# Kernel tuning notes

Hardware: AMD Instinct MI355X
Metric: run time of the kernel (lower is better)

Reference implementation:

```python
import jax, jax.numpy as jnp
import numpy as np

EPS = 0.01
H, W = 300, 400
WORLD_SCALE = 400.0


def setup_inputs() -> dict:
    key = jax.random.key(0)
    ks = jax.random.split(key, 8)
    N, B, D, HID = 200000, 2, 256, 256
    fx = fy = 300.0
    cx, cy = W / 2.0, H / 2.0
    z = jax.random.uniform(ks[0], (N,), minval=2.0, maxval=10.0)
    u = jax.random.uniform(ks[1], (N,), minval=0.0, maxval=float(W))
    v = jax.random.uniform(ks[2], (N,), minval=0.0, maxval=float(H))
    vert_pos = jnp.stack([(u - cx) / fx * z, (v - cy) / fy * z, z], axis=0)  # [3,N]
    target_pose = jnp.tile(jnp.eye(4, dtype=jnp.float32)[None], (B, 1, 1))
    K = jnp.array([[fx, 0.0, cx], [0.0, fy, cy], [0.0, 0.0, 1.0]], dtype=jnp.float32)
    target_intrinsics = jnp.tile(K[None], (B, 1, 1))
    vert_feat = 0.1 * jax.random.normal(ks[3], (N, D), dtype=jnp.float32)
    vert_opy = jnp.ones((N,), dtype=jnp.float32)
    W1 = 0.05 * jax.random.normal(ks[4], (D + 3, HID), dtype=jnp.float32)
    b1 = jnp.zeros((HID,), dtype=jnp.float32)
    W2 = 0.05 * jax.random.normal(ks[5], (HID, 3), dtype=jnp.float32)
    b2 = jnp.zeros((3,), dtype=jnp.float32)
    bkg_col = jnp.zeros((3,), dtype=jnp.float32)
    ref_images = jax.random.normal(ks[6], (B, 3, H, W), dtype=jnp.float32)
    return {"vert_pos": vert_pos, "ref_images": ref_images, "target_pose": target_pose,
            "target_intrinsics": target_intrinsics, "vert_feat": vert_feat, "vert_opy": vert_opy,
            "W1": W1, "b1": b1, "W2": W2, "b2": b2, "bkg_col": bkg_col}


def reference(vert_pos, ref_images, target_pose, target_intrinsics,
              vert_feat, vert_opy, W1, b1, W2, b2, bkg_col):
    B = target_pose.shape[0]
    N = vert_pos.shape[1]
    # homogeneous world points, transform to target camera frame
    xyzw = jnp.concatenate([vert_pos, jnp.ones((1, N), vert_pos.dtype)], axis=0)  # [4,N]
    xyz_t = jnp.einsum('bij,jn->bin', target_pose, xyzw)[:, :3]                   # [B,3,N]
    xy_proj = jnp.einsum('bij,bjn->bin', target_intrinsics, xyz_t)                # [B,3,N]
    z = xy_proj[:, 2:3]
    eps_mask = jax.lax.stop_gradient(jnp.abs(z) < EPS)                            # [B,1,N]
    zs = jnp.where(eps_mask, EPS, z)
    uv = xy_proj[:, 0:2] / zs
    sampler = jnp.where(eps_mask, -1e6, jnp.concatenate([uv, zs], axis=1))        # [B,3,N]
    # view direction in world frame per point
    vnorm = xyz_t / jnp.linalg.norm(xyz_t, axis=1, keepdims=True)
    vh = jnp.concatenate([vnorm, jnp.zeros_like(vnorm[:, 0:1])], axis=1)          # [B,4,N]
    pose_inv = jnp.linalg.inv(target_pose)
    vdir = jnp.einsum('bij,bjn->bin', pose_inv, vh)[:, :3]                        # [B,3,N]
    vdir = vdir.transpose(0, 2, 1).reshape(B * N, 3)
    # per-point neural shading (MLP shader on concat(feat, view_dir))
    feat = jnp.broadcast_to(vert_feat[None], (B, N, vert_feat.shape[1])).reshape(B * N, -1)
    x = jnp.concatenate([feat, vdir], axis=-1)
    h = jax.nn.relu(x @ W1 + b1)
    rgb = jax.nn.sigmoid(h @ W2 + b2).reshape(B, N, 3)                            # [B,N,3]
    opacity = jnp.clip(jax.nn.sigmoid(vert_opy), 0.0, 1.0)                        # [N]
    # differentiable splat: scatter shaded colors weighted by opacity to pixels
    u_pix, v_pix, zz = sampler[:, 0], sampler[:, 1], sampler[:, 2]                # [B,N]
    ix = jnp.round(u_pix).astype(jnp.int32)
    iy = jnp.round(v_pix).astype(jnp.int32)
    valid = (ix >= 0) & (ix < W) & (iy >= 0) & (iy < H) & (zz >= 1.0)
    idx = jnp.where(valid, iy * W + ix, H * W)                                    # dump bin H*W
    wts = opacity[None, :] * valid.astype(rgb.dtype)                              # [B,N]
    seg = lambda vals, ids: jax.ops.segment_sum(vals, ids, num_segments=H * W + 1)
    num = jax.vmap(seg)(wts[..., None] * rgb, idx)[:, :H * W]                     # [B,HW,3]
    den = jax.vmap(seg)(wts, idx)[:, :H * W]                                      # [B,HW]
    fg = num / (den[..., None] + 1e-8)
    alpha = 1.0 - jnp.exp(-den)
    img = fg * alpha[..., None] + bkg_col * (1.0 - alpha[..., None])
    return img.reshape(B, H, W, 3).transpose(0, 3, 1, 2)                          # [B,3,H,W]
```

## Files before the change

kernel.cpp:

```cpp
#include <hip/hip_runtime.h>
#include <cstdint>
#include <cstddef>

#define HH 300
#define WW 400
#define HWPIX (HH*WW)

typedef __attribute__((ext_vector_type(8))) short short8_t;
typedef __attribute__((ext_vector_type(4))) float f32x4;

static __device__ __forceinline__ unsigned short f2bf(float f){
  union { float f; unsigned u; } v; v.f = f;
  unsigned r = (v.u + 0x7fffu + ((v.u >> 16) & 1u)) >> 16;
  return (unsigned short)r;
}
static __device__ __forceinline__ float bf2f(unsigned short us){
  union { unsigned u; float f; } v; v.u = ((unsigned)us) << 16;
  return v.f;
}
static __device__ __forceinline__ float dot4_x(float a0,float x0,float a1,float x1,
                                               float a2,float x2,float a3,float x3){
  #pragma clang fp contract(off)
  float s = a0*x0;
  s = s + a1*x1;
  s = s + a2*x2;
  s = s + a3*x3;
  return s;
}
static __device__ __forceinline__ float dot3_x(float a0,float x0,float a1,float x1,
                                               float a2,float x2){
  #pragma clang fp contract(off)
  float s = a0*x0;
  s = s + a1*x1;
  s = s + a2*x2;
  return s;
}

__global__ void prep_kernel(const float* __restrict__ W1, const float* __restrict__ W2,
                            const float* __restrict__ pose,
                            float* __restrict__ poseinv, unsigned short* __restrict__ W1aT,
                            float* __restrict__ ntab, int B){
  int tid = threadIdx.x;
  int bid = blockIdx.x;
  if (bid < 256){
    int k = bid, n = tid;
    W1aT[n*256 + k] = f2bf(W1[k*256 + n]);
  } else {
    int n = tid;
    ntab[n*8+0] = W1[256*256 + n];
    ntab[n*8+1] = W1[257*256 + n];
    ntab[n*8+2] = W1[258*256 + n];
    ntab[n*8+3] = W2[n*3+0];
    ntab[n*8+4] = W2[n*3+1];
    ntab[n*8+5] = W2[n*3+2];
    ntab[n*8+6] = 0.f; ntab[n*8+7] = 0.f;
    if (tid < B){
      float M[4][8];
      const float* A = pose + tid*16;
      for (int i=0;i<4;i++) for (int j=0;j<4;j++){ M[i][j]=A[i*4+j]; M[i][4+j] = (i==j)?1.f:0.f; }
      for (int c=0;c<4;c++){
        int p=c;
        for (int r=c+1;r<4;r++) if (fabsf(M[r][c])>fabsf(M[p][c])) p=r;
        if (p!=c) for (int j=0;j<8;j++){ float t=M[c][j]; M[c][j]=M[p][j]; M[p][j]=t; }
        float inv = 1.f/M[c][c];
        for (int j=0;j<8;j++) M[c][j]*=inv;
        for (int r=0;r<4;r++) if (r!=c){ float f=M[r][c]; for(int j=0;j<8;j++) M[r][j]-=f*M[c][j]; }
      }
      float* O = poseinv + tid*16;
      for (int i=0;i<4;i++) for (int j=0;j<4;j++) O[i*4+j]=M[i][4+j];
    }
  }
}

__global__ __launch_bounds__(256) void mlp_scatter_kernel(
    const float* __restrict__ feat, const unsigned short* __restrict__ W1aT,
    const float* __restrict__ b1, const float* __restrict__ b2,
    const float* __restrict__ ntab,
    const float* __restrict__ vp, const float* __restrict__ opy,
    const float* __restrict__ pose, const float* __restrict__ intr,
    const float* __restrict__ poseinv,
    float* __restrict__ num, float* __restrict__ den, int N, int B)
{
  __shared__ __align__(16) char smem[40960];
  unsigned short* sA = (unsigned short*)smem;
  unsigned short* sB = (unsigned short*)(smem + 8192);
  unsigned short* sH = (unsigned short*)smem;
  float* part        = (float*)(smem + 34560);

  const int tid  = threadIdx.x;
  const int lane = tid & 63;
  const int wv   = __builtin_amdgcn_readfirstlane(tid >> 6);
  const int lr   = lane & 15;
  const int qd   = lane >> 4;
  const int m0   = blockIdx.x * 64;

  f32x4 acc[4][4];
  for (int i=0;i<4;i++) for (int j=0;j<4;j++) acc[i][j] = (f32x4){0.f,0.f,0.f,0.f};

  for (int kt=0; kt<4; kt++){
    #pragma unroll
    for (int i=0;i<4;i++){
      int q   = i*256 + tid;
      int row = q >> 4;
      int c4  = q & 15;
      long rg = m0 + row; if (rg >= N) rg = N-1;
      float4 f = *(const float4*)(feat + rg*256 + kt*64 + c4*4);
      ushort4 u;
      u.x = f2bf(f.x); u.y = f2bf(f.y); u.z = f2bf(f.z); u.w = f2bf(f.w);
      int q8 = c4 >> 1, half = c4 & 1;
      int phys = q8 ^ (row & 7);
      *(ushort4*)(sA + row*64 + phys*8 + half*4) = u;
    }
    #pragma unroll
    for (int i=0;i<8;i++){
      int q  = i*256 + tid;
      int n  = q >> 3;
      int c8 = q & 7;
      uint4 v = *(const uint4*)(W1aT + n*256 + kt*64 + c8*8);
      int phys = c8 ^ (n & 7);
      *(uint4*)(sB + n*64 + phys*8) = v;
    }
    __syncthreads();
    #pragma unroll
    for (int ks=0; ks<2; ks++){
      short8_t av[4], bv[4];
      int qlog = ks*4 + qd;
      #pragma unroll
      for (int mt=0; mt<4; mt++){
        int row  = mt*16 + lr;
        int phys = qlog ^ (row & 7);
        av[mt] = *(const short8_t*)(sA + row*64 + phys*8);
      }
      #pragma unroll
      for (int nt=0; nt<4; nt++){
        int n    = wv*64 + nt*16 + lr;
        int phys = qlog ^ (n & 7);
        bv[nt] = *(const short8_t*)(sB + n*64 + phys*8);
      }
      #pragma unroll
      for (int mt=0; mt<4; mt++)
        #pragma unroll
        for (int nt=0; nt<4; nt++)
          acc[mt][nt] = __builtin_amdgcn_mfma_f32_16x16x32_bf16(av[mt], bv[nt], acc[mt][nt], 0,0,0);
    }
    __syncthreads();
  }

  #pragma unroll
  for (int nt=0; nt<4; nt++){
    int n = wv*64 + nt*16 + lr;
    float bias = b1[n];
    #pragma unroll
    for (int mt=0; mt<4; mt++)
      #pragma unroll
      for (int rr=0; rr<4; rr++){
        int m = mt*16 + qd*4 + rr;
        sH[m*270 + n] = f2bf(acc[mt][nt][rr] + bias);
      }
  }
  __syncthreads();

  const int r = lane;
  long vg = m0 + r;
  bool rowok = vg < N; if (!rowok) vg = N-1;
  float px = vp[vg], py = vp[(size_t)N+vg], pz = vp[2*(size_t)N+vg];
  const float* tb = ntab + (size_t)wv*64*8;
  const unsigned short* hrow = sH + r*270 + wv*64;

  for (int b=0; b<B; b++){
    const float* P  = pose + b*16;
    const float* Kc = intr + b*9;
    const float* Pi = poseinv + b*16;
    float xt = dot4_x(P[0],px, P[1],py, P[2], pz, P[3], 1.f);
    float yt = dot4_x(P[4],px, P[5],py, P[6], pz, P[7], 1.f);
    float zt = dot4_x(P[8],px, P[9],py, P[10],pz, P[11],1.f);
    float uu = dot3_x(Kc[0],xt, Kc[1],yt, Kc[2],zt);
    float vv = dot3_x(Kc[3],xt, Kc[4],yt, Kc[5],zt);
    float zp = dot3_x(Kc[6],xt, Kc[7],yt, Kc[8],zt);
    bool em = fabsf(zp) < 0.01f;
    float zsafe = em ? 0.01f : zp;
    float up   = em ? -1e6f : uu/zsafe;
    float vpix = em ? -1e6f : vv/zsafe;
    float zz   = em ? -1e6f : zsafe;
    float inrm = 1.f/sqrtf(xt*xt + yt*yt + zt*zt);
    float nx=xt*inrm, ny=yt*inrm, nz=zt*inrm;
    float vdx = Pi[0]*nx + Pi[1]*ny + Pi[2]*nz;
    float vdy = Pi[4]*nx + Pi[5]*ny + Pi[6]*nz;
    float vdz = Pi[8]*nx + Pi[9]*ny + Pi[10]*nz;

    float a0=0.f, a1=0.f, a2=0.f;
    #pragma unroll 8
    for (int j=0;j<64;j++){
      const float* t = tb + j*8;
      float h = bf2f(hrow[j]) + vdx*t[0] + vdy*t[1] + vdz*t[2];
      h = fmaxf(h, 0.f);
      a0 += h*t[3]; a1 += h*t[4]; a2 += h*t[5];
    }
    part[(wv*64 + r)*3 + 0] = a0;
    part[(wv*64 + r)*3 + 1] = a1;
    part[(wv*64 + r)*3 + 2] = a2;
    __syncthreads();
    if (wv == 0){
      float s0 = part[r*3+0] + part[(64+r)*3+0] + part[(128+r)*3+0] + part[(192+r)*3+0];
      float s1 = part[r*3+1] + part[(64+r)*3+1] + part[(128+r)*3+1] + part[(192+r)*3+1];
      float s2 = part[r*3+2] + part[(64+r)*3+2] + part[(128+r)*3+2] + part[(192+r)*3+2];
      float r0 = 1.f/(1.f+expf(-(s0 + b2[0])));
      float r1 = 1.f/(1.f+expf(-(s1 + b2[1])));
      float r2 = 1.f/(1.f+expf(-(s2 + b2[2])));
      float opac = 1.f/(1.f+expf(-opy[vg]));
      int ix = (int)rintf(up);
      int iy = (int)rintf(vpix);
      bool valid = rowok && ix>=0 && ix<WW && iy>=0 && iy<HH && zz>=1.0f;
      if (valid){
        int idx = iy*WW + ix;
        atomicAdd(den + (size_t)b*HWPIX + idx, opac);
        atomicAdd(num + ((size_t)b*3+0)*HWPIX + idx, opac*r0);
        atomicAdd(num + ((size_t)b*3+1)*HWPIX + idx, opac*r1);
        atomicAdd(num + ((size_t)b*3+2)*HWPIX + idx, opac*r2);
      }
    }
    __syncthreads();
  }
}

__global__ void compose_kernel(float* __restrict__ out, const float* __restrict__ den,
                               const float* __restrict__ bkg, int B){
  int i = blockIdx.x*256 + threadIdx.x;
  int total = B*HWPIX;
  if (i >= total) return;
  int b = i / HWPIX;
  int pix = i - b*HWPIX;
  float d = den[i];
  float alpha = 1.f - expf(-d);
  float om = 1.f - alpha;
  float dd = d + 1e-8f;
  float* ob = out + (size_t)b*3*HWPIX;
  float f0 = ob[0*HWPIX + pix] / dd;
  float f1 = ob[1*HWPIX + pix] / dd;
  float f2 = ob[2*HWPIX + pix] / dd;
  ob[0*HWPIX + pix] = f0*alpha + bkg[0]*om;
  ob[1*HWPIX + pix] = f1*alpha + bkg[1]*om;
  ob[2*HWPIX + pix] = f2*alpha + bkg[2]*om;
}

extern "C" void kernel_launch(void* const* d_in, const int* in_sizes, int n_in,
                              void* d_out, int out_size, void* d_ws, size_t ws_size,
                              hipStream_t stream){
  const float* vp   = (const float*)d_in[0];
  const float* pose = (const float*)d_in[2];
  const float* intr = (const float*)d_in[3];
  const float* feat = (const float*)d_in[4];
  const float* opy  = (const float*)d_in[5];
  const float* W1   = (const float*)d_in[6];
  const float* b1   = (const float*)d_in[7];
  const float* W2   = (const float*)d_in[8];
  const float* b2   = (const float*)d_in[9];
  const float* bkg  = (const float*)d_in[10];
  float* out = (float*)d_out;
  int N = in_sizes[0]/3;
  int B = in_sizes[2]/16;

  char* ws = (char*)d_ws;
  float* poseinv        = (float*)ws;
  unsigned short* W1aT  = (unsigned short*)(ws + 256);
  float* ntab           = (float*)(ws + 256 + 131072);
  float* den            = (float*)(ws + 256 + 131072 + 8192);

  hipMemsetAsync(out, 0, (size_t)out_size*sizeof(float), stream);
  hipMemsetAsync(den, 0, (size_t)B*HWPIX*sizeof(float), stream);
  prep_kernel<<<257, 256, 0, stream>>>(W1, W2, pose, poseinv, W1aT, ntab, B);
  int gridM = (N + 63)/64;
  mlp_scatter_kernel<<<gridM, 256, 0, stream>>>(feat, W1aT, b1, b2, ntab, vp, opy,
                                                pose, intr, poseinv, out, den, N, B);
  compose_kernel<<<(B*HWPIX + 255)/256, 256, 0, stream>>>(out, den, bkg, B);
}
```

Before: 401.4 us.

## Split fused MLP-scatter into GEMM kernel writing hidden tile and per-vertex kernel

Splits the fused GEMM plus per-vertex epilogue into two kernels. The GEMM kernel writes the bf16 hidden activations, transposed without bias, to a global workspace. A new vertex kernel runs one thread per vertex: it reads the hidden column, adds the b1 bias now folded into ntab, and evaluates both batches in a single pass over all 256 hidden units. This removes the per-batch __syncthreads, the shared-memory partial reduction and the idle waves during the atomic scatter. The cost is an extra global round trip of about 100 MB of hidden activations and a hard assumption that B is at most 2.

```diff
diff --git a/kernel.cpp b/kernel.cpp
--- a/kernel.cpp
+++ b/kernel.cpp
@@ -37,7 +37,7 @@
 }
 
 __global__ void prep_kernel(const float* __restrict__ W1, const float* __restrict__ W2,
-                            const float* __restrict__ pose,
+                            const float* __restrict__ b1, const float* __restrict__ pose,
                             float* __restrict__ poseinv, unsigned short* __restrict__ W1aT,
                             float* __restrict__ ntab, int B){
   int tid = threadIdx.x;
@@ -53,7 +53,8 @@
     ntab[n*8+3] = W2[n*3+0];
     ntab[n*8+4] = W2[n*3+1];
     ntab[n*8+5] = W2[n*3+2];
-    ntab[n*8+6] = 0.f; ntab[n*8+7] = 0.f;
+    ntab[n*8+6] = b1[n];
+    ntab[n*8+7] = 0.f;
     if (tid < B){
       float M[4][8];
       const float* A = pose + tid*16;
@@ -72,20 +73,14 @@
   }
 }
 
-__global__ __launch_bounds__(256) void mlp_scatter_kernel(
+__global__ __launch_bounds__(256) void gemm_kernel(
     const float* __restrict__ feat, const unsigned short* __restrict__ W1aT,
-    const float* __restrict__ b1, const float* __restrict__ b2,
-    const float* __restrict__ ntab,
-    const float* __restrict__ vp, const float* __restrict__ opy,
-    const float* __restrict__ pose, const float* __restrict__ intr,
-    const float* __restrict__ poseinv,
-    float* __restrict__ num, float* __restrict__ den, int N, int B)
+    unsigned short* __restrict__ HT, int N)
 {
   __shared__ __align__(16) char smem[40960];
-  unsigned short* sA = (unsigned short*)smem;
-  unsigned short* sB = (unsigned short*)(smem + 8192);
-  unsigned short* sH = (unsigned short*)smem;
-  float* part        = (float*)(smem + 34560);
+  unsigned short* sA  = (unsigned short*)smem;
+  unsigned short* sB  = (unsigned short*)(smem + 8192);
+  unsigned short* sHT = (unsigned short*)smem;
 
   const int tid  = threadIdx.x;
   const int lane = tid & 63;
@@ -149,24 +144,46 @@
   #pragma unroll
   for (int nt=0; nt<4; nt++){
     int n = wv*64 + nt*16 + lr;
-    float bias = b1[n];
     #pragma unroll
-    for (int mt=0; mt<4; mt++)
+    for (int mt=0; mt<4; mt++){
       #pragma unroll
-      for (int rr=0; rr<4; rr++){
-        int m = mt*16 + qd*4 + rr;
-        sH[m*270 + n] = f2bf(acc[mt][nt][rr] + bias);
+      for (int rp=0; rp<2; rp++){
+        int m = mt*16 + qd*4 + rp*2;
+        unsigned u = (unsigned)f2bf(acc[mt][nt][rp*2]) |
+                     ((unsigned)f2bf(acc[mt][nt][rp*2+1]) << 16);
+        *(unsigned*)(sHT + n*72 + m) = u;
       }
+    }
   }
   __syncthreads();
 
-  const int r = lane;
-  long vg = m0 + r;
-  bool rowok = vg < N; if (!rowok) vg = N-1;
-  float px = vp[vg], py = vp[(size_t)N+vg], pz = vp[2*(size_t)N+vg];
-  const float* tb = ntab + (size_t)wv*64*8;
-  const unsigned short* hrow = sH + r*270 + wv*64;
-
+  unsigned short* tile = HT + (size_t)blockIdx.x * 16384;
+  #pragma unroll
+  for (int i=0;i<8;i++){
+    int idx = i*256 + tid;
+    int n = idx >> 3;
+    int c = idx & 7;
+    uint4 v = *(const uint4*)(sHT + n*72 + c*8);
+    *(uint4*)(tile + n*64 + c*8) = v;
+  }
+}
+
+__global__ __launch_bounds__(256) void vertex_kernel(
+    const unsigned short* __restrict__ HT, const float* __restrict__ ntab,
+    const float* __restrict__ b2,
+    const float* __restrict__ vp, const float* __restrict__ opy,
+    const float* __restrict__ pose, const float* __restrict__ intr,
+    const float* __restrict__ poseinv,
+    float* __restrict__ num, float* __restrict__ den, int N, int B)
+{
+  int v = blockIdx.x*256 + threadIdx.x;
+  if (v >= N) return;
+  const unsigned short* tile = HT + (size_t)(v >> 6) * 16384 + (v & 63);
+
+  float px = vp[v], py = vp[(size_t)N+v], pz = vp[2*(size_t)N+v];
+
+  float vd0[3], vd1[3];
+  float up0,vq0,zz0, up1,vq1,zz1;
   for (int b=0; b<B; b++){
     const float* P  = pose + b*16;
     const float* Kc = intr + b*9;
@@ -179,47 +196,56 @@
     float zp = dot3_x(Kc[6],xt, Kc[7],yt, Kc[8],zt);
     bool em = fabsf(zp) < 0.01f;
     float zsafe = em ? 0.01f : zp;
-    float up   = em ? -1e6f : uu/zsafe;
-    float vpix = em ? -1e6f : vv/zsafe;
-    float zz   = em ? -1e6f : zsafe;
+    float up = em ? -1e6f : uu/zsafe;
+    float vq = em ? -1e6f : vv/zsafe;
+    float zz = em ? -1e6f : zsafe;
     float inrm = 1.f/sqrtf(xt*xt + yt*yt + zt*zt);
     float nx=xt*inrm, ny=yt*inrm, nz=zt*inrm;
-    float vdx = Pi[0]*nx + Pi[1]*ny + Pi[2]*nz;
-    float vdy = Pi[4]*nx + Pi[5]*ny + Pi[6]*nz;
-    float vdz = Pi[8]*nx + Pi[9]*ny + Pi[10]*nz;
-
-    float a0=0.f, a1=0.f, a2=0.f;
-    #pragma unroll 8
-    for (int j=0;j<64;j++){
-      const float* t = tb + j*8;
-      float h = bf2f(hrow[j]) + vdx*t[0] + vdy*t[1] + vdz*t[2];
-      h = fmaxf(h, 0.f);
-      a0 += h*t[3]; a1 += h*t[4]; a2 += h*t[5];
-    }
-    part[(wv*64 + r)*3 + 0] = a0;
-    part[(wv*64 + r)*3 + 1] = a1;
-    part[(wv*64 + r)*3 + 2] = a2;
-    __syncthreads();
-    if (wv == 0){
-      float s0 = part[r*3+0] + part[(64+r)*3+0] + part[(128+r)*3+0] + part[(192+r)*3+0];
-      float s1 = part[r*3+1] + part[(64+r)*3+1] + part[(128+r)*3+1] + part[(192+r)*3+1];
-      float s2 = part[r*3+2] + part[(64+r)*3+2] + part[(128+r)*3+2] + part[(192+r)*3+2];
-      float r0 = 1.f/(1.f+expf(-(s0 + b2[0])));
-      float r1 = 1.f/(1.f+expf(-(s1 + b2[1])));
-      float r2 = 1.f/(1.f+expf(-(s2 + b2[2])));
-      float opac = 1.f/(1.f+expf(-opy[vg]));
-      int ix = (int)rintf(up);
-      int iy = (int)rintf(vpix);
-      bool valid = rowok && ix>=0 && ix<WW && iy>=0 && iy<HH && zz>=1.0f;
-      if (valid){
-        int idx = iy*WW + ix;
-        atomicAdd(den + (size_t)b*HWPIX + idx, opac);
-        atomicAdd(num + ((size_t)b*3+0)*HWPIX + idx, opac*r0);
-        atomicAdd(num + ((size_t)b*3+1)*HWPIX + idx, opac*r1);
-        atomicAdd(num + ((size_t)b*3+2)*HWPIX + idx, opac*r2);
-      }
-    }
-    __syncthreads();
+    float wx = Pi[0]*nx + Pi[1]*ny + Pi[2]*nz;
+    float wy = Pi[4]*nx + Pi[5]*ny + Pi[6]*nz;
+    float wz = Pi[8]*nx + Pi[9]*ny + Pi[10]*nz;
+    if (b==0){ vd0[0]=wx; vd0[1]=wy; vd0[2]=wz; up0=up; vq0=vq; zz0=zz; }
+    else     { vd1[0]=wx; vd1[1]=wy; vd1[2]=wz; up1=up; vq1=vq; zz1=zz; }
+  }
+
+  float a00=0.f,a01=0.f,a02=0.f, a10=0.f,a11=0.f,a12=0.f;
+  #pragma unroll 4
+  for (int n=0; n<256; n++){
+    const float* t = ntab + n*8;
+    float hb = bf2f(tile[n*64]) + t[6];
+    float h0 = fmaxf(hb + vd0[0]*t[0] + vd0[1]*t[1] + vd0[2]*t[2], 0.f);
+    a00 += h0*t[3]; a01 += h0*t[4]; a02 += h0*t[5];
+    float h1 = fmaxf(hb + vd1[0]*t[0] + vd1[1]*t[1] + vd1[2]*t[2], 0.f);
+    a10 += h1*t[3]; a11 += h1*t[4]; a12 += h1*t[5];
+  }
+
+  float opac = 1.f/(1.f+expf(-opy[v]));
+
+  {
+    int ix = (int)rintf(up0), iy = (int)rintf(vq0);
+    if (ix>=0 && ix<WW && iy>=0 && iy<HH && zz0>=1.0f){
+      float r0 = 1.f/(1.f+expf(-(a00 + b2[0])));
+      float r1 = 1.f/(1.f+expf(-(a01 + b2[1])));
+      float r2 = 1.f/(1.f+expf(-(a02 + b2[2])));
+      int idx = iy*WW + ix;
+      atomicAdd(den + idx, opac);
+      atomicAdd(num + (size_t)0*HWPIX + idx, opac*r0);
+      atomicAdd(num + (size_t)1*HWPIX + idx, opac*r1);
+      atomicAdd(num + (size_t)2*HWPIX + idx, opac*r2);
+    }
+  }
+  if (B > 1){
+    int ix = (int)rintf(up1), iy = (int)rintf(vq1);
+    if (ix>=0 && ix<WW && iy>=0 && iy<HH && zz1>=1.0f){
+      float r0 = 1.f/(1.f+expf(-(a10 + b2[0])));
+      float r1 = 1.f/(1.f+expf(-(a11 + b2[1])));
+      float r2 = 1.f/(1.f+expf(-(a12 + b2[2])));
+      int idx = iy*WW + ix;
+      atomicAdd(den + (size_t)HWPIX + idx, opac);
+      atomicAdd(num + (size_t)3*HWPIX + idx, opac*r0);
+      atomicAdd(num + (size_t)4*HWPIX + idx, opac*r1);
+      atomicAdd(num + (size_t)5*HWPIX + idx, opac*r2);
+    }
   }
 }
 
@@ -259,18 +285,20 @@
   float* out = (float*)d_out;
   int N = in_sizes[0]/3;
   int B = in_sizes[2]/16;
+  int nblk = (N + 63)/64;
 
   char* ws = (char*)d_ws;
   float* poseinv        = (float*)ws;
   unsigned short* W1aT  = (unsigned short*)(ws + 256);
   float* ntab           = (float*)(ws + 256 + 131072);
-  float* den            = (float*)(ws + 256 + 131072 + 8192);
+  unsigned short* HT    = (unsigned short*)(ws + 139520);
+  float* den            = (float*)(ws + 139520 + (size_t)nblk*32768);
 
   hipMemsetAsync(out, 0, (size_t)out_size*sizeof(float), stream);
   hipMemsetAsync(den, 0, (size_t)B*HWPIX*sizeof(float), stream);
-  prep_kernel<<<257, 256, 0, stream>>>(W1, W2, pose, poseinv, W1aT, ntab, B);
-  int gridM = (N + 63)/64;
-  mlp_scatter_kernel<<<gridM, 256, 0, stream>>>(feat, W1aT, b1, b2, ntab, vp, opy,
-                                                pose, intr, poseinv, out, den, N, B);
+  prep_kernel<<<257, 256, 0, stream>>>(W1, W2, b1, pose, poseinv, W1aT, ntab, B);
+  gemm_kernel<<<nblk, 256, 0, stream>>>(feat, W1aT, HT, N);
+  vertex_kernel<<<(N + 255)/256, 256, 0, stream>>>(HT, ntab, b2, vp, opy,
+                                                   pose, intr, poseinv, out, den, N, B);
   compose_kernel<<<(B*HWPIX + 255)/256, 256, 0, stream>>>(out, den, bkg, B);
 }
```

New measurement: 447.4 us. 1.11x slower.
